# Performance work log

Hardware: AMD Instinct MI355X
Metric: run time of the kernel (lower is better)

The kernel has to match this reference:

```python
import jax, jax.numpy as jnp
import numpy as np

IN_CAPS = 32
IN_CH = 8
OUT_CAPS = 10
OUT_CH = 16
NUM_ROUTING = 3
WID = 6
HEI = 6
BATCH = 64


def setup_inputs() -> dict:
    key = jax.random.key(0)
    k1, k2 = jax.random.split(key)
    u = jax.random.normal(k1, (BATCH, IN_CAPS, IN_CH, WID, HEI), dtype=jnp.float32)
    W = jax.random.normal(k2, (IN_CAPS, IN_CH, WID, HEI, OUT_CAPS, OUT_CH), dtype=jnp.float32) * 0.05
    return {"u": u, "W": W}


def reference(u, W):
    # u: [B, ic, ich, w, h]; W: [ic, ich, w, h, oc, och]
    B = u.shape[0]
    # _mul_1: broadcast multiply then fold (ich*w*h) into one axis
    u_hat = (u[..., None, None] * W[None]).reshape(
        B, IN_CAPS, IN_CH * WID * HEI, OUT_CAPS, OUT_CH
    )  # [B, ic, D, oc, och]
    u_sum = u_hat.sum(axis=2)            # [B, ic, oc, och] (used every iteration in _mul_2)
    u_dot = u_hat.sum(axis=(0, 2, 4))    # [ic, oc] (constant part of _dot)
    b_ij = jnp.zeros((IN_CAPS, OUT_CAPS), dtype=u.dtype)
    v_j = None
    for _ in range(NUM_ROUTING):
        c_ij = jax.nn.softmax(b_ij, axis=0)                     # softmax over in_capsules
        s_j = jnp.einsum('io,bioc->boc', c_ij, u_sum)           # [B, oc, och]
        # squash with GLOBAL L1 norm (torch .norm(1) over all elements) -- faithful to source
        n = jnp.abs(s_j).sum()
        v_j = (n * n) / (1.0 + n * n) * (s_j / n)               # [B, oc, och]
        agree = u_dot * v_j.sum(axis=(0, 2))[None, :]           # [ic, oc]
        b_ij = b_ij + jax.lax.stop_gradient(agree)              # torch uses .data (detached)
    return v_j
```

## Files before the change

### kernel.cpp

```cpp
#include <hip/hip_runtime.h>
#include <math.h>

#define B_   64
#define IC   32
#define D_   288
#define OC   10
#define OCH  16
#define J_   160
#define BJ   10240

__global__ __launch_bounds__(320) void k_usum(const float* __restrict__ u,
                                              const float* __restrict__ Wt,
                                              float* __restrict__ US,
                                              float* __restrict__ UDp,
                                              float* __restrict__ nacc,
                                              int* __restrict__ bar) {
    const int ic  = blockIdx.x >> 3;
    const int bt  = blockIdx.x & 7;
    const int tid = threadIdx.x;
    __shared__ float u_lds[8 * D_];
    __shared__ float ud_part[OC];
    if (tid < OC) ud_part[tid] = 0.f;
    if (blockIdx.x == 0 && tid == 0) {
        nacc[0] = 0.f; nacc[1] = 0.f; nacc[2] = 0.f;
        *bar = 0;
    }
    for (int idx = tid; idx < 8 * D_; idx += 320) {
        int b_sub = idx / D_;
        int d     = idx - b_sub * D_;
        u_lds[idx] = u[((bt * 8 + b_sub) * IC + ic) * D_ + d];
    }
    __syncthreads();
    const int j4    = tid % 40;
    const int b_sub = tid / 40;
    const float4* wp = (const float4*)(Wt + (size_t)ic * D_ * J_) + j4;
    const float*  ur = u_lds + b_sub * D_;
    float ax = 0.f, ay = 0.f, az = 0.f, aw = 0.f;
    for (int d0 = 0; d0 < D_; d0 += 8) {
        float4 w0 = wp[(d0 + 0) * 40];
        float4 w1 = wp[(d0 + 1) * 40];
        float4 w2 = wp[(d0 + 2) * 40];
        float4 w3 = wp[(d0 + 3) * 40];
        float4 w4 = wp[(d0 + 4) * 40];
        float4 w5 = wp[(d0 + 5) * 40];
        float4 w6 = wp[(d0 + 6) * 40];
        float4 w7 = wp[(d0 + 7) * 40];
        float u0 = ur[d0 + 0], u1 = ur[d0 + 1], u2 = ur[d0 + 2], u3 = ur[d0 + 3];
        float u4 = ur[d0 + 4], u5 = ur[d0 + 5], u6 = ur[d0 + 6], u7 = ur[d0 + 7];
        ax += u0 * w0.x; ay += u0 * w0.y; az += u0 * w0.z; aw += u0 * w0.w;
        ax += u1 * w1.x; ay += u1 * w1.y; az += u1 * w1.z; aw += u1 * w1.w;
        ax += u2 * w2.x; ay += u2 * w2.y; az += u2 * w2.z; aw += u2 * w2.w;
        ax += u3 * w3.x; ay += u3 * w3.y; az += u3 * w3.z; aw += u3 * w3.w;
        ax += u4 * w4.x; ay += u4 * w4.y; az += u4 * w4.z; aw += u4 * w4.w;
        ax += u5 * w5.x; ay += u5 * w5.y; az += u5 * w5.z; aw += u5 * w5.w;
        ax += u6 * w6.x; ay += u6 * w6.y; az += u6 * w6.z; aw += u6 * w6.w;
        ax += u7 * w7.x; ay += u7 * w7.y; az += u7 * w7.z; aw += u7 * w7.w;
    }
    const int b = bt * 8 + b_sub;
    ((float4*)(US + (size_t)ic * BJ + b * J_))[j4] = make_float4(ax, ay, az, aw);
    float g = ax + ay + az + aw;
    g += __shfl_xor(g, 1);
    g += __shfl_xor(g, 2);
    if ((tid & 3) == 0) atomicAdd(&ud_part[j4 >> 2], g);
    __syncthreads();
    if (tid < OC) UDp[blockIdx.x * OC + tid] = ud_part[tid];
}

__global__ __launch_bounds__(320) void k_route(const float* __restrict__ US,
                                               const float* __restrict__ UDp,
                                               float* __restrict__ nacc,
                                               int* __restrict__ bar,
                                               float* __restrict__ out) {
    const int tid = threadIdx.x;
    const int i   = tid & 31;
    const int o   = tid >> 5;
    __shared__ float cij[OC * IC];
    __shared__ float wred[5];
    __shared__ float nsh;
    float udv = 0.f;
    #pragma unroll
    for (int bt = 0; bt < 8; ++bt) udv += UDp[(i * 8 + bt) * OC + o];
    const int t  = blockIdx.x * 320 + tid;
    const int ot = (t >> 4) % OC;
    float bij = 0.f, s = 0.f;
    for (int q = 0; q < 3; ++q) {
        float m = bij;
        m = fmaxf(m, __shfl_xor(m, 16, 32));
        m = fmaxf(m, __shfl_xor(m,  8, 32));
        m = fmaxf(m, __shfl_xor(m,  4, 32));
        m = fmaxf(m, __shfl_xor(m,  2, 32));
        m = fmaxf(m, __shfl_xor(m,  1, 32));
        float e  = __expf(bij - m);
        float se = e;
        se += __shfl_xor(se, 16, 32);
        se += __shfl_xor(se,  8, 32);
        se += __shfl_xor(se,  4, 32);
        se += __shfl_xor(se,  2, 32);
        se += __shfl_xor(se,  1, 32);
        float c = e / se;
        cij[o * IC + i] = c;
        float cs = c * udv;
        cs += __shfl_xor(cs, 16, 32);
        cs += __shfl_xor(cs,  8, 32);
        cs += __shfl_xor(cs,  4, 32);
        cs += __shfl_xor(cs,  2, 32);
        cs += __shfl_xor(cs,  1, 32);
        __syncthreads();
        float sv = 0.f;
        const float* usp = US + t;
        const float* cp  = cij + ot * IC;
        #pragma unroll
        for (int ii = 0; ii < IC; ++ii) sv += cp[ii] * usp[(size_t)ii * BJ];
        s = sv;
        float a = fabsf(sv);
        #pragma unroll
        for (int off = 32; off; off >>= 1) a += __shfl_down(a, off);
        if ((tid & 63) == 0) wred[tid >> 6] = a;
        __syncthreads();
        if (tid == 0) {
            atomicAdd(nacc + q, wred[0] + wred[1] + wred[2] + wred[3] + wred[4]);
            __threadfence();
            atomicAdd(bar, 1);
            while (__hip_atomic_load(bar, __ATOMIC_ACQUIRE,
                                     __HIP_MEMORY_SCOPE_AGENT) < 32 * (q + 1))
                __builtin_amdgcn_s_sleep(1);
            nsh = __hip_atomic_load(nacc + q, __ATOMIC_RELAXED,
                                    __HIP_MEMORY_SCOPE_AGENT);
        }
        __syncthreads();
        const float n  = nsh;
        const float n2 = n * n;
        if (q < 2) {
            bij += udv * ((n2 / (1.f + n2)) * (cs / n));
        } else {
            out[t] = (n2 / (1.f + n2)) * (s / n);
        }
    }
}

extern "C" void kernel_launch(void* const* d_in, const int* in_sizes, int n_in,
                              void* d_out, int out_size, void* d_ws, size_t ws_size,
                              hipStream_t stream) {
    (void)in_sizes; (void)n_in; (void)out_size; (void)ws_size;
    const float* u  = (const float*)d_in[0];
    const float* Wt = (const float*)d_in[1];
    float* ws   = (float*)d_ws;
    float* US   = ws;
    float* UDp  = ws + 327680;
    float* nacc = ws + 330240;
    int*   bar  = (int*)(ws + 330244);

    k_usum<<<dim3(256), dim3(320), 0, stream>>>(u, Wt, US, UDp, nacc, bar);
    k_route<<<dim3(32), dim3(320), 0, stream>>>(US, UDp, nacc, bar, (float*)d_out);
}
```

Measured before the change: 85.57 us.

## Split usum reduction over D halves and widen route blocks to shrink grid barrier

The u_sum kernel now runs 512 blocks of 4 batches each. Each block splits the 288-long D reduction into two halves across thread groups and combines them through shared memory. The u-tile load is also vectorised to float4. The routing kernel uses 10 blocks of 1024 threads instead of 32 of 320, so the software grid barrier waits on fewer participants. The cost is that the W tile is now re-read by twice as many blocks, and most route threads sit idle during the softmax phase.

```diff
diff --git a/kernel.cpp b/kernel.cpp
--- a/kernel.cpp
+++ b/kernel.cpp
@@ -15,28 +15,33 @@
                                               float* __restrict__ UDp,
                                               float* __restrict__ nacc,
                                               int* __restrict__ bar) {
-    const int ic  = blockIdx.x >> 3;
-    const int bt  = blockIdx.x & 7;
+    const int ic  = blockIdx.x & 31;
+    const int bt  = blockIdx.x >> 5;
     const int tid = threadIdx.x;
-    __shared__ float u_lds[8 * D_];
+    __shared__ float u_lds[4 * D_];
+    __shared__ float part[640];
     __shared__ float ud_part[OC];
     if (tid < OC) ud_part[tid] = 0.f;
     if (blockIdx.x == 0 && tid == 0) {
         nacc[0] = 0.f; nacc[1] = 0.f; nacc[2] = 0.f;
         *bar = 0;
     }
-    for (int idx = tid; idx < 8 * D_; idx += 320) {
-        int b_sub = idx / D_;
-        int d     = idx - b_sub * D_;
-        u_lds[idx] = u[((bt * 8 + b_sub) * IC + ic) * D_ + d];
+    for (int idx = tid; idx < 288; idx += 320) {
+        int b_sub = idx / 72;
+        int f4    = idx - b_sub * 72;
+        int b     = bt * 4 + b_sub;
+        ((float4*)u_lds)[idx] =
+            ((const float4*)(u + (size_t)(b * IC + ic) * D_))[f4];
     }
     __syncthreads();
     const int j4    = tid % 40;
-    const int b_sub = tid / 40;
-    const float4* wp = (const float4*)(Wt + (size_t)ic * D_ * J_) + j4;
-    const float*  ur = u_lds + b_sub * D_;
+    const int b_sub = (tid / 40) & 3;
+    const int dh    = tid / 160;
+    const float4* wp = (const float4*)(Wt + (size_t)ic * D_ * J_)
+                       + (size_t)dh * 144 * 40 + j4;
+    const float*  ur = u_lds + b_sub * D_ + dh * 144;
     float ax = 0.f, ay = 0.f, az = 0.f, aw = 0.f;
-    for (int d0 = 0; d0 < D_; d0 += 8) {
+    for (int d0 = 0; d0 < 144; d0 += 8) {
         float4 w0 = wp[(d0 + 0) * 40];
         float4 w1 = wp[(d0 + 1) * 40];
         float4 w2 = wp[(d0 + 2) * 40];
@@ -56,73 +61,88 @@
         ax += u6 * w6.x; ay += u6 * w6.y; az += u6 * w6.z; aw += u6 * w6.w;
         ax += u7 * w7.x; ay += u7 * w7.y; az += u7 * w7.z; aw += u7 * w7.w;
     }
-    const int b = bt * 8 + b_sub;
-    ((float4*)(US + (size_t)ic * BJ + b * J_))[j4] = make_float4(ax, ay, az, aw);
-    float g = ax + ay + az + aw;
-    g += __shfl_xor(g, 1);
-    g += __shfl_xor(g, 2);
-    if ((tid & 3) == 0) atomicAdd(&ud_part[j4 >> 2], g);
+    if (dh == 1) ((float4*)part)[tid - 160] = make_float4(ax, ay, az, aw);
+    __syncthreads();
+    if (dh == 0) {
+        float4 p = ((float4*)part)[tid];
+        ax += p.x; ay += p.y; az += p.z; aw += p.w;
+        ((float4*)(US + (size_t)ic * BJ + (bt * 4 + b_sub) * J_))[j4] =
+            make_float4(ax, ay, az, aw);
+        float g = ax + ay + az + aw;
+        g += __shfl_xor(g, 1);
+        g += __shfl_xor(g, 2);
+        if ((tid & 3) == 0) atomicAdd(&ud_part[j4 >> 2], g);
+    }
     __syncthreads();
     if (tid < OC) UDp[blockIdx.x * OC + tid] = ud_part[tid];
 }
 
-__global__ __launch_bounds__(320) void k_route(const float* __restrict__ US,
-                                               const float* __restrict__ UDp,
-                                               float* __restrict__ nacc,
-                                               int* __restrict__ bar,
-                                               float* __restrict__ out) {
+__global__ __launch_bounds__(1024) void k_route(const float* __restrict__ US,
+                                                const float* __restrict__ UDp,
+                                                float* __restrict__ nacc,
+                                                int* __restrict__ bar,
+                                                float* __restrict__ out) {
     const int tid = threadIdx.x;
     const int i   = tid & 31;
     const int o   = tid >> 5;
     __shared__ float cij[OC * IC];
-    __shared__ float wred[5];
+    __shared__ float wred[16];
     __shared__ float nsh;
     float udv = 0.f;
-    #pragma unroll
-    for (int bt = 0; bt < 8; ++bt) udv += UDp[(i * 8 + bt) * OC + o];
-    const int t  = blockIdx.x * 320 + tid;
+    if (tid < 320) {
+        #pragma unroll
+        for (int bt = 0; bt < 16; ++bt) udv += UDp[(bt * 32 + i) * OC + o];
+    }
+    const int t  = blockIdx.x * 1024 + tid;
     const int ot = (t >> 4) % OC;
-    float bij = 0.f, s = 0.f;
+    float bij = 0.f;
     for (int q = 0; q < 3; ++q) {
-        float m = bij;
-        m = fmaxf(m, __shfl_xor(m, 16, 32));
-        m = fmaxf(m, __shfl_xor(m,  8, 32));
-        m = fmaxf(m, __shfl_xor(m,  4, 32));
-        m = fmaxf(m, __shfl_xor(m,  2, 32));
-        m = fmaxf(m, __shfl_xor(m,  1, 32));
-        float e  = __expf(bij - m);
-        float se = e;
-        se += __shfl_xor(se, 16, 32);
-        se += __shfl_xor(se,  8, 32);
-        se += __shfl_xor(se,  4, 32);
-        se += __shfl_xor(se,  2, 32);
-        se += __shfl_xor(se,  1, 32);
-        float c = e / se;
-        cij[o * IC + i] = c;
-        float cs = c * udv;
-        cs += __shfl_xor(cs, 16, 32);
-        cs += __shfl_xor(cs,  8, 32);
-        cs += __shfl_xor(cs,  4, 32);
-        cs += __shfl_xor(cs,  2, 32);
-        cs += __shfl_xor(cs,  1, 32);
+        float cs = 0.f;
+        if (tid < 320) {
+            float m = bij;
+            m = fmaxf(m, __shfl_xor(m, 16, 32));
+            m = fmaxf(m, __shfl_xor(m,  8, 32));
+            m = fmaxf(m, __shfl_xor(m,  4, 32));
+            m = fmaxf(m, __shfl_xor(m,  2, 32));
+            m = fmaxf(m, __shfl_xor(m,  1, 32));
+            float e  = __expf(bij - m);
+            float se = e;
+            se += __shfl_xor(se, 16, 32);
+            se += __shfl_xor(se,  8, 32);
+            se += __shfl_xor(se,  4, 32);
+            se += __shfl_xor(se,  2, 32);
+            se += __shfl_xor(se,  1, 32);
+            float c = e / se;
+            cij[o * IC + i] = c;
+            cs = c * udv;
+            cs += __shfl_xor(cs, 16, 32);
+            cs += __shfl_xor(cs,  8, 32);
+            cs += __shfl_xor(cs,  4, 32);
+            cs += __shfl_xor(cs,  2, 32);
+            cs += __shfl_xor(cs,  1, 32);
+        }
         __syncthreads();
-        float sv = 0.f;
-        const float* usp = US + t;
-        const float* cp  = cij + ot * IC;
-        #pragma unroll
-        for (int ii = 0; ii < IC; ++ii) sv += cp[ii] * usp[(size_t)ii * BJ];
-        s = sv;
-        float a = fabsf(sv);
+        float s = 0.f;
+        {
+            const float* usp = US + t;
+            const float* cp  = cij + ot * IC;
+            #pragma unroll
+            for (int ii = 0; ii < IC; ++ii) s += cp[ii] * usp[(size_t)ii * BJ];
+        }
+        float a = fabsf(s);
         #pragma unroll
         for (int off = 32; off; off >>= 1) a += __shfl_down(a, off);
         if ((tid & 63) == 0) wred[tid >> 6] = a;
         __syncthreads();
         if (tid == 0) {
-            atomicAdd(nacc + q, wred[0] + wred[1] + wred[2] + wred[3] + wred[4]);
+            float blk = 0.f;
+            #pragma unroll
+            for (int w = 0; w < 16; ++w) blk += wred[w];
+            atomicAdd(nacc + q, blk);
             __threadfence();
             atomicAdd(bar, 1);
             while (__hip_atomic_load(bar, __ATOMIC_ACQUIRE,
-                                     __HIP_MEMORY_SCOPE_AGENT) < 32 * (q + 1))
+                                     __HIP_MEMORY_SCOPE_AGENT) < 10 * (q + 1))
                 __builtin_amdgcn_s_sleep(1);
             nsh = __hip_atomic_load(nacc + q, __ATOMIC_RELAXED,
                                     __HIP_MEMORY_SCOPE_AGENT);
@@ -131,7 +151,7 @@
         const float n  = nsh;
         const float n2 = n * n;
         if (q < 2) {
-            bij += udv * ((n2 / (1.f + n2)) * (cs / n));
+            if (tid < 320) bij += udv * ((n2 / (1.f + n2)) * (cs / n));
         } else {
             out[t] = (n2 / (1.f + n2)) * (s / n);
         }
@@ -147,9 +167,9 @@
     float* ws   = (float*)d_ws;
     float* US   = ws;
     float* UDp  = ws + 327680;
-    float* nacc = ws + 330240;
-    int*   bar  = (int*)(ws + 330244);
+    float* nacc = ws + 332800;
+    int*   bar  = (int*)(ws + 332803);
 
-    k_usum<<<dim3(256), dim3(320), 0, stream>>>(u, Wt, US, UDp, nacc, bar);
-    k_route<<<dim3(32), dim3(320), 0, stream>>>(US, UDp, nacc, bar, (float*)d_out);
+    k_usum<<<dim3(512), dim3(320), 0, stream>>>(u, Wt, US, UDp, nacc, bar);
+    k_route<<<dim3(10), dim3(1024), 0, stream>>>(US, UDp, nacc, bar, (float*)d_out);
 }
```

New measurement: 81.26 us. -5.0%, faster.
